# Optimization experiments

Measured on AMD Instinct MI355X. Metric: run time of the kernel, lower is better.

The kernel has to match this reference:

```python
import jax, jax.numpy as jnp
import numpy as np

BITWIDTH = 4  # sqllm 4-bit packing: 8 codes per int32


def sqllm_dequant4(qweight, lut):
    # qweight: [num_int32s, N] int32 (stored packed); lut: [N, 16]
    qw = qweight.T  # [N, num_int32s]
    shifts = jnp.arange(8, dtype=jnp.int32) * 4  # [8]
    # extract 8 nibbles per int32 -> indices in [0, 16)
    idx = (qw[:, :, None] >> shifts[None, None, :]) & 15  # [N, num_int32s, 8]
    N = qw.shape[0]
    idx = idx.reshape(N, -1)  # [N, K] with K = num_int32s * 8
    return jnp.take_along_axis(lut, idx, axis=1)  # [N, K]


def setup_inputs() -> dict:
    key = jax.random.key(0)
    k1, k2, k3 = jax.random.split(key, 3)
    B, S, K, N = 4, 2048, 4096, 4096
    inp = {
        "input": jax.random.normal(k1, (B, S, K), dtype=jnp.float32),
        "qweight": jax.random.randint(k2, (K // 8, N), 0, 2147483647, dtype=jnp.int32),
        "lut": jax.random.normal(k3, (N, 16), dtype=jnp.float32),
    }
    return inp


def reference(input, qweight, lut):
    # sqllm_gemm: dequantize packed 4-bit weights via LUT gather, then input @ W.T
    weights = sqllm_dequant4(qweight, lut)  # [N, K]
    return jnp.einsum("bsk,nk->bsn", input, weights)  # [B, S, N]
```

## Files before the change

### kernel.cpp

```cpp
#include <hip/hip_runtime.h>
#include <hip/hip_bf16.h>


typedef __attribute__((ext_vector_type(4))) float  f32x4;
typedef __attribute__((ext_vector_type(4))) int    i32x4;
typedef __attribute__((ext_vector_type(8))) short  bf16x8;

__device__ __forceinline__ unsigned short f2bf(float f) {
    __hip_bfloat16 h = __float2bfloat16(f);
    return __builtin_bit_cast(unsigned short, h);
}

__device__ __forceinline__ void gload16(const unsigned short* g, unsigned short* l) {
    __builtin_amdgcn_global_load_lds(
        (const __attribute__((address_space(1))) unsigned int*)g,
        (__attribute__((address_space(3))) unsigned int*)l, 16, 0, 0);
}


__global__ void convA_kernel(const float* __restrict__ in, unsigned short* __restrict__ o, long n8) {
    long i = (long)blockIdx.x * blockDim.x + threadIdx.x;
    long stride = (long)gridDim.x * blockDim.x;
    const f32x4* in4 = reinterpret_cast<const f32x4*>(in);
    bf16x8* o8 = reinterpret_cast<bf16x8*>(o);
    for (; i < n8; i += stride) {
        f32x4 a = in4[2 * i];
        f32x4 b = in4[2 * i + 1];
        bf16x8 e;
#pragma unroll
        for (int x = 0; x < 4; ++x) {
            e[x]     = (short)f2bf(a[x]);
            e[4 + x] = (short)f2bf(b[x]);
        }
        o8[i] = e;
    }
}

__global__ void dequantW_kernel(const int* __restrict__ Q, const float* __restrict__ lut,
                                unsigned short* __restrict__ Wb, int N, long total) {
    long i = (long)blockIdx.x * blockDim.x + threadIdx.x;
    if (i >= total) return;
    unsigned int v = (unsigned int)Q[i];
    int n = (int)(i % N);
    const float* lp = lut + (long)n * 16;
    bf16x8 w;
#pragma unroll
    for (int p = 0; p < 8; ++p)
        w[p] = (short)f2bf(lp[(v >> (4 * p)) & 15]);
    reinterpret_cast<bf16x8*>(Wb)[i] = w;
}


__global__ __launch_bounds__(512, 2)
void gemm8p(const unsigned short* __restrict__ Abf, const unsigned short* __restrict__ Wb,
            float* __restrict__ out, int M, int N, int K) {
    __shared__ __align__(16) unsigned short sA[4 * 8192];
    __shared__ __align__(16) unsigned short sB[4 * 8192];

    const int tid  = threadIdx.x;
    const int lane = tid & 63;
    const int wid  = tid >> 6;
    const int wr   = wid >> 2;
    const int wc   = wid & 3;
    const int r15  = lane & 15;
    const int hi   = lane >> 4;

    int nwg = gridDim.x, orig = blockIdx.x;
    int wg = ((nwg & 7) == 0) ? (orig & 7) * (nwg >> 3) + (orig >> 3) : orig;
    const int NBN = N / 256;
    const int m0 = (wg / NBN) * 256, n0 = (wg % NBN) * 256;

    const int NH = K / 32;

    const int aoff = (wr * 128 + r15) * 32 + ((hi ^ ((r15 >> 1) & 3)) << 3);
    const int boff = hi * 2048 + (wc * 64 + r15) * 8;

    auto stage = [&](int S, int slot) {
#pragma unroll
        for (int j = 0; j < 2; ++j) {
            int idx = j * 512 + tid;
            int m = idx >> 2, kc = idx & 3;
            const unsigned short* srcA = Abf + (size_t)(m0 + m) * K + S * 32
                                         + ((kc ^ ((m >> 1) & 3)) << 3);
            gload16(srcA, sA + slot * 8192 + j * 4096 + wid * 512);
            int kc2 = idx >> 8, n = idx & 255;
            const unsigned short* srcB = Wb + ((size_t)(S * 4 + kc2) * N + n0 + n) * 8;
            gload16(srcB, sB + slot * 8192 + j * 4096 + wid * 512);
        }
    };

    f32x4 acc[8][4] = {};

    stage(0, 0);
    stage(1, 1);
    stage(2, 2);
    asm volatile("s_waitcnt vmcnt(8)" ::: "memory");
    __builtin_amdgcn_s_barrier();

#define PHASE(U) do {                                                             \
    const unsigned short* SA = sA + (U) * 8192;                                   \
    const unsigned short* SB = sB + (U) * 8192;                                   \
    bf16x8 av[8], bv[4];                                                          \
    _Pragma("unroll") for (int nf = 0; nf < 4; ++nf)                              \
        bv[nf] = *(const bf16x8*)(SB + boff + nf * 128);                          \
    _Pragma("unroll") for (int mf = 0; mf < 8; ++mf)                              \
        av[mf] = *(const bf16x8*)(SA + aoff + mf * 512);                          \
    int S = H + (U) + 3; if (S >= NH) S -= NH;                                    \
    stage(S, ((U) + 3) & 3);                                                      \
    asm volatile("s_waitcnt vmcnt(8)" ::: "memory");                              \
    __builtin_amdgcn_s_barrier();                                                 \
    __builtin_amdgcn_s_setprio(1);                                                \
    _Pragma("unroll") for (int mf = 0; mf < 8; ++mf)                              \
        _Pragma("unroll") for (int nf = 0; nf < 4; ++nf)                          \
            acc[mf][nf] = __builtin_amdgcn_mfma_f32_16x16x32_bf16(                \
                av[mf], bv[nf], acc[mf][nf], 0, 0, 0);                            \
    __builtin_amdgcn_s_setprio(0);                                                \
    __builtin_amdgcn_s_barrier();                                                 \
} while (0)

    for (int H = 0; H < NH; H += 4) {
        PHASE(0);
        PHASE(1);
        PHASE(2);
        PHASE(3);
    }
#undef PHASE

    asm volatile("s_waitcnt vmcnt(0)" ::: "memory");

#pragma unroll
    for (int mf = 0; mf < 8; ++mf) {
        const int mrow = m0 + wr * 128 + mf * 16 + hi * 4;
#pragma unroll
        for (int nf = 0; nf < 4; ++nf) {
            const int ncol = n0 + wc * 64 + nf * 16 + r15;
            float* po = out + (size_t)mrow * N + ncol;
#pragma unroll
            for (int r = 0; r < 4; ++r) po[(size_t)r * N] = acc[mf][nf][r];
        }
    }
}


#define FBM 128
#define FBN 128
#define FBK 64

__device__ __forceinline__ int fswz(int row, int kb) {
    return row * (FBK * 2) + (kb ^ ((row & 7) << 4));
}

__global__ __launch_bounds__(256, 2)
void sqllm_gemm_fused(const float* __restrict__ A, const int* __restrict__ Q,
                      const float* __restrict__ lut, float* __restrict__ out,
                      int M, int N, int K) {
    __shared__ __align__(16) char sA[FBM * FBK * 2];
    __shared__ __align__(16) char sB[FBN * FBK * 2];
    __shared__ float sLut[FBN * 17];

    const int tid  = threadIdx.x;
    const int lane = tid & 63;
    const int wid  = tid >> 6;
    const int wr   = wid >> 1;
    const int wc   = wid & 1;
    const int n0 = blockIdx.x * FBN;
    const int m0 = blockIdx.y * FBM;

    for (int i = tid; i < FBN * 16; i += 256) {
        int n = i >> 4, c = i & 15;
        sLut[n * 17 + c] = lut[(long)(n0 + n) * 16 + c];
    }
    __syncthreads();

    f32x4 acc[4][4] = {};
    const int nK = K / FBK;
    for (int kk = 0; kk < nK; ++kk) {
        {
            const int r = tid >> 1, h = tid & 1;
            const float* ap = A + (long)(m0 + r) * K + kk * FBK + h * 32;
            f32x4 v[8];
#pragma unroll
            for (int j = 0; j < 8; ++j) v[j] = reinterpret_cast<const f32x4*>(ap)[j];
            const int kr = tid >> 5, nq = (tid & 31) << 2;
            const int* qp = Q + (long)(kk * (FBK / 8) + kr) * N + n0 + nq;
            i32x4 q = *reinterpret_cast<const i32x4*>(qp);
#pragma unroll
            for (int j = 0; j < 4; ++j) {
                bf16x8 e;
#pragma unroll
                for (int x = 0; x < 4; ++x) {
                    e[x]     = (short)f2bf(v[2 * j][x]);
                    e[4 + x] = (short)f2bf(v[2 * j + 1][x]);
                }
                *reinterpret_cast<bf16x8*>(sA + fswz(r, h * 64 + j * 16)) = e;
            }
#pragma unroll
            for (int c = 0; c < 4; ++c) {
                const int n = nq + c;
                const float* lp = sLut + n * 17;
                unsigned int qq = (unsigned int)q[c];
                bf16x8 w;
#pragma unroll
                for (int p = 0; p < 8; ++p)
                    w[p] = (short)f2bf(lp[(qq >> (4 * p)) & 15]);
                *reinterpret_cast<bf16x8*>(sB + fswz(n, kr * 16)) = w;
            }
        }
        __syncthreads();
#pragma unroll
        for (int kh = 0; kh < 2; ++kh) {
            const int kb = kh * 64 + (lane >> 4) * 16;
            bf16x8 af[4], bfv[4];
#pragma unroll
            for (int i = 0; i < 4; ++i) {
                af[i]  = *reinterpret_cast<const bf16x8*>(sA + fswz(wr * 64 + i * 16 + (lane & 15), kb));
                bfv[i] = *reinterpret_cast<const bf16x8*>(sB + fswz(wc * 64 + i * 16 + (lane & 15), kb));
            }
#pragma unroll
            for (int i = 0; i < 4; ++i)
#pragma unroll
                for (int j = 0; j < 4; ++j)
                    acc[i][j] = __builtin_amdgcn_mfma_f32_16x16x32_bf16(af[i], bfv[j], acc[i][j], 0, 0, 0);
        }
        __syncthreads();
    }
    const int col = lane & 15;
    const int r4  = (lane >> 4) * 4;
#pragma unroll
    for (int i = 0; i < 4; ++i) {
        const int mrow = m0 + wr * 64 + i * 16 + r4;
#pragma unroll
        for (int j = 0; j < 4; ++j) {
            const int ncol = n0 + wc * 64 + j * 16 + col;
#pragma unroll
            for (int r = 0; r < 4; ++r)
                out[(long)(mrow + r) * N + ncol] = acc[i][j][r];
        }
    }
}

extern "C" void kernel_launch(void* const* d_in, const int* in_sizes, int n_in,
                              void* d_out, int out_size, void* d_ws, size_t ws_size,
                              hipStream_t stream) {
    const float* A   = (const float*)d_in[0];
    const int*   Q   = (const int*)d_in[1];
    const float* lut = (const float*)d_in[2];
    float* out = (float*)d_out;

    const long szA = in_sizes[0], szQ = in_sizes[1], szL = in_sizes[2];
    const int N = (int)(szL / 16);
    const int K = (int)(szQ * 8 / N);
    const int M = (int)(szA / K);

    const size_t needA = (size_t)M * K * 2;
    const size_t needW = (size_t)K * N * 2;

    const bool shape_ok = (M % 256 == 0) && (N % 256 == 0) && (K % 128 == 0);

    if (shape_ok && ws_size >= needA + needW) {
        unsigned short* Abf = (unsigned short*)d_ws;
        unsigned short* Wb  = (unsigned short*)((char*)d_ws + needA);
        const long n8 = (long)M * K / 8;
        convA_kernel<<<2048, 256, 0, stream>>>(A, Abf, n8);
        const long tq = (long)(K / 8) * N;
        dequantW_kernel<<<(int)((tq + 255) / 256), 256, 0, stream>>>(Q, lut, Wb, N, tq);
        dim3 grid((M / 256) * (N / 256));
        gemm8p<<<grid, 512, 0, stream>>>(Abf, Wb, out, M, N, K);
    } else {
        dim3 grid(N / FBN, M / FBM);
        sqllm_gemm_fused<<<grid, 256, 0, stream>>>(A, Q, lut, out, M, N, K);
    }
}
```

Baseline: 299.5 us.

## Interleave LDS fragment loads with MFMAs and drop mid-phase barrier

Precomputes per-thread global source and LDS destination pointers so each stage issue is four loads with simple offsets instead of recomputed index math. The phase body now issues the next stage's prefetch first, then interleaves the A-fragment LDS reads with the MFMA groups so that matrix ops start before all fragments are loaded. It also removes one of the two barriers per phase by moving the vmcnt wait and single barrier to the end. This lowers register pressure and address-arithmetic overhead, but relies on the 4-slot ring leaving enough distance that dropping the barrier does not create LDS read/write races.

```diff
diff --git a/kernel.cpp b/kernel.cpp
--- a/kernel.cpp
+++ b/kernel.cpp
@@ -51,6 +51,12 @@
 }
 
 
+#define MFMA4(MF, AF) \
+    acc[MF][0] = __builtin_amdgcn_mfma_f32_16x16x32_bf16(AF, bv0, acc[MF][0], 0, 0, 0); \
+    acc[MF][1] = __builtin_amdgcn_mfma_f32_16x16x32_bf16(AF, bv1, acc[MF][1], 0, 0, 0); \
+    acc[MF][2] = __builtin_amdgcn_mfma_f32_16x16x32_bf16(AF, bv2, acc[MF][2], 0, 0, 0); \
+    acc[MF][3] = __builtin_amdgcn_mfma_f32_16x16x32_bf16(AF, bv3, acc[MF][3], 0, 0, 0);
+
 __global__ __launch_bounds__(512, 2)
 void gemm8p(const unsigned short* __restrict__ Abf, const unsigned short* __restrict__ Wb,
             float* __restrict__ out, int M, int N, int K) {
@@ -75,18 +81,22 @@
     const int aoff = (wr * 128 + r15) * 32 + ((hi ^ ((r15 >> 1) & 3)) << 3);
     const int boff = hi * 2048 + (wc * 64 + r15) * 8;
 
+    const int am  = tid >> 2, akc = tid & 3;
+    const int akcs = (akc ^ ((am >> 1) & 3)) << 3;
+    const unsigned short* baseA0 = Abf + (size_t)(m0 + am) * K + akcs;
+    const unsigned short* baseA1 = Abf + (size_t)(m0 + am + 128) * K + akcs;
+    const int bkc = tid >> 8, bn = tid & 255;
+    const unsigned short* baseB0 = Wb + ((size_t)bkc * N + n0 + bn) * 8;
+    const unsigned short* baseB1 = Wb + ((size_t)(bkc + 2) * N + n0 + bn) * 8;
+    const size_t bstride = (size_t)32 * N;
+    unsigned short* const dA = sA + wid * 512;
+    unsigned short* const dB = sB + wid * 512;
+
     auto stage = [&](int S, int slot) {
-#pragma unroll
-        for (int j = 0; j < 2; ++j) {
-            int idx = j * 512 + tid;
-            int m = idx >> 2, kc = idx & 3;
-            const unsigned short* srcA = Abf + (size_t)(m0 + m) * K + S * 32
-                                         + ((kc ^ ((m >> 1) & 3)) << 3);
-            gload16(srcA, sA + slot * 8192 + j * 4096 + wid * 512);
-            int kc2 = idx >> 8, n = idx & 255;
-            const unsigned short* srcB = Wb + ((size_t)(S * 4 + kc2) * N + n0 + n) * 8;
-            gload16(srcB, sB + slot * 8192 + j * 4096 + wid * 512);
-        }
+        gload16(baseA0 + S * 32, dA + slot * 8192);
+        gload16(baseB0 + S * bstride, dB + slot * 8192);
+        gload16(baseA1 + S * 32, dA + slot * 8192 + 4096);
+        gload16(baseB1 + S * bstride, dB + slot * 8192 + 4096);
     };
 
     f32x4 acc[8][4] = {};
@@ -100,21 +110,31 @@
 #define PHASE(U) do {                                                             \
     const unsigned short* SA = sA + (U) * 8192;                                   \
     const unsigned short* SB = sB + (U) * 8192;                                   \
-    bf16x8 av[8], bv[4];                                                          \
-    _Pragma("unroll") for (int nf = 0; nf < 4; ++nf)                              \
-        bv[nf] = *(const bf16x8*)(SB + boff + nf * 128);                          \
-    _Pragma("unroll") for (int mf = 0; mf < 8; ++mf)                              \
-        av[mf] = *(const bf16x8*)(SA + aoff + mf * 512);                          \
     int S = H + (U) + 3; if (S >= NH) S -= NH;                                    \
     stage(S, ((U) + 3) & 3);                                                      \
+    bf16x8 bv0 = *(const bf16x8*)(SB + boff + 0 * 128);                           \
+    bf16x8 bv1 = *(const bf16x8*)(SB + boff + 1 * 128);                           \
+    bf16x8 bv2 = *(const bf16x8*)(SB + boff + 2 * 128);                           \
+    bf16x8 bv3 = *(const bf16x8*)(SB + boff + 3 * 128);                           \
+    bf16x8 a0 = *(const bf16x8*)(SA + aoff + 0 * 512);                            \
+    bf16x8 a1 = *(const bf16x8*)(SA + aoff + 1 * 512);                            \
+    __builtin_amdgcn_s_setprio(1);                                                \
+    bf16x8 a2 = *(const bf16x8*)(SA + aoff + 2 * 512);                            \
+    bf16x8 a3 = *(const bf16x8*)(SA + aoff + 3 * 512);                            \
+    MFMA4(0, a0)                                                                  \
+    MFMA4(1, a1)                                                                  \
+    bf16x8 a4 = *(const bf16x8*)(SA + aoff + 4 * 512);                            \
+    bf16x8 a5 = *(const bf16x8*)(SA + aoff + 5 * 512);                            \
+    MFMA4(2, a2)                                                                  \
+    MFMA4(3, a3)                                                                  \
+    bf16x8 a6 = *(const bf16x8*)(SA + aoff + 6 * 512);                            \
+    bf16x8 a7 = *(const bf16x8*)(SA + aoff + 7 * 512);                            \
+    MFMA4(4, a4)                                                                  \
+    MFMA4(5, a5)                                                                  \
+    MFMA4(6, a6)                                                                  \
+    MFMA4(7, a7)                                                                  \
+    __builtin_amdgcn_s_setprio(0);                                                \
     asm volatile("s_waitcnt vmcnt(8)" ::: "memory");                              \
-    __builtin_amdgcn_s_barrier();                                                 \
-    __builtin_amdgcn_s_setprio(1);                                                \
-    _Pragma("unroll") for (int mf = 0; mf < 8; ++mf)                              \
-        _Pragma("unroll") for (int nf = 0; nf < 4; ++nf)                          \
-            acc[mf][nf] = __builtin_amdgcn_mfma_f32_16x16x32_bf16(                \
-                av[mf], bv[nf], acc[mf][nf], 0, 0, 0);                            \
-    __builtin_amdgcn_s_setprio(0);                                                \
     __builtin_amdgcn_s_barrier();                                                 \
 } while (0)
 
```

New measurement: 295.7 us. No clear change (-1.3%).

## Replace 256x256 GEMM tile with 256x128 tile, 4 waves, triple-buffered pipeline

Applied to the files above, without the earlier changes.

The main bf16 GEMM moves from 512-thread blocks with 256x256 output tiles and a 4-slot LDS ring to 256-thread blocks with 256x128 tiles and a 3-slot ring. The K loop is now a single rolled loop with one barrier per step instead of two, and global load addresses are precomputed outside the loop. The aim is lower LDS use and sync overhead and more blocks in flight. The trade-off is that a smaller N tile lowers reuse of A per block, so more A traffic goes to global memory.

```diff
diff --git a/kernel.cpp b/kernel.cpp
--- a/kernel.cpp
+++ b/kernel.cpp
@@ -51,80 +51,87 @@
 }
 
 
-__global__ __launch_bounds__(512, 2)
-void gemm8p(const unsigned short* __restrict__ Abf, const unsigned short* __restrict__ Wb,
+__global__ __launch_bounds__(256, 2)
+void gemm2b(const unsigned short* __restrict__ Abf, const unsigned short* __restrict__ Wb,
             float* __restrict__ out, int M, int N, int K) {
-    __shared__ __align__(16) unsigned short sA[4 * 8192];
-    __shared__ __align__(16) unsigned short sB[4 * 8192];
+    __shared__ __align__(16) unsigned short sA[3 * 8192];
+    __shared__ __align__(16) unsigned short sB[3 * 4096];
 
     const int tid  = threadIdx.x;
     const int lane = tid & 63;
     const int wid  = tid >> 6;
-    const int wr   = wid >> 2;
-    const int wc   = wid & 3;
+    const int wr   = wid >> 1;
+    const int wc   = wid & 1;
     const int r15  = lane & 15;
     const int hi   = lane >> 4;
 
+    const int NBN = N / 128;
     int nwg = gridDim.x, orig = blockIdx.x;
     int wg = ((nwg & 7) == 0) ? (orig & 7) * (nwg >> 3) + (orig >> 3) : orig;
-    const int NBN = N / 256;
-    const int m0 = (wg / NBN) * 256, n0 = (wg % NBN) * 256;
+    const int m0 = (wg / NBN) * 256, n0 = (wg % NBN) * 128;
 
     const int NH = K / 32;
 
     const int aoff = (wr * 128 + r15) * 32 + ((hi ^ ((r15 >> 1) & 3)) << 3);
-    const int boff = hi * 2048 + (wc * 64 + r15) * 8;
+    const int boff = hi * 1024 + (wc * 64 + r15) * 8;
+
+    const int am  = tid >> 2, akc = tid & 3;
+    const int akcs = (akc ^ ((am >> 1) & 3)) << 3;
+    const unsigned short* baseA = Abf + (size_t)(m0 + am) * K + akcs;
+    const size_t ajump = (size_t)64 * K;
+    const int bn = tid & 127, bk0 = tid >> 7;
+    const unsigned short* baseB0 = Wb + ((size_t)bk0 * N + n0 + bn) * 8;
+    const unsigned short* baseB1 = Wb + ((size_t)(bk0 + 2) * N + n0 + bn) * 8;
+    const size_t bstride = (size_t)32 * N;
+    unsigned short* const dA = sA + wid * 512;
+    unsigned short* const dB = sB + wid * 512;
 
     auto stage = [&](int S, int slot) {
-#pragma unroll
-        for (int j = 0; j < 2; ++j) {
-            int idx = j * 512 + tid;
-            int m = idx >> 2, kc = idx & 3;
-            const unsigned short* srcA = Abf + (size_t)(m0 + m) * K + S * 32
-                                         + ((kc ^ ((m >> 1) & 3)) << 3);
-            gload16(srcA, sA + slot * 8192 + j * 4096 + wid * 512);
-            int kc2 = idx >> 8, n = idx & 255;
-            const unsigned short* srcB = Wb + ((size_t)(S * 4 + kc2) * N + n0 + n) * 8;
-            gload16(srcB, sB + slot * 8192 + j * 4096 + wid * 512);
-        }
+        const unsigned short* a = baseA + (size_t)S * 32;
+        unsigned short* da = dA + slot * 8192;
+#pragma unroll
+        for (int j = 0; j < 4; ++j)
+            gload16(a + j * ajump, da + j * 2048);
+        gload16(baseB0 + S * bstride, dB + slot * 4096);
+        gload16(baseB1 + S * bstride, dB + slot * 4096 + 2048);
     };
 
     f32x4 acc[8][4] = {};
 
     stage(0, 0);
     stage(1, 1);
-    stage(2, 2);
-    asm volatile("s_waitcnt vmcnt(8)" ::: "memory");
+    asm volatile("s_waitcnt vmcnt(6)" ::: "memory");
     __builtin_amdgcn_s_barrier();
 
-#define PHASE(U) do {                                                             \
-    const unsigned short* SA = sA + (U) * 8192;                                   \
-    const unsigned short* SB = sB + (U) * 8192;                                   \
-    bf16x8 av[8], bv[4];                                                          \
-    _Pragma("unroll") for (int nf = 0; nf < 4; ++nf)                              \
-        bv[nf] = *(const bf16x8*)(SB + boff + nf * 128);                          \
-    _Pragma("unroll") for (int mf = 0; mf < 8; ++mf)                              \
-        av[mf] = *(const bf16x8*)(SA + aoff + mf * 512);                          \
-    int S = H + (U) + 3; if (S >= NH) S -= NH;                                    \
-    stage(S, ((U) + 3) & 3);                                                      \
-    asm volatile("s_waitcnt vmcnt(8)" ::: "memory");                              \
-    __builtin_amdgcn_s_barrier();                                                 \
-    __builtin_amdgcn_s_setprio(1);                                                \
-    _Pragma("unroll") for (int mf = 0; mf < 8; ++mf)                              \
-        _Pragma("unroll") for (int nf = 0; nf < 4; ++nf)                          \
-            acc[mf][nf] = __builtin_amdgcn_mfma_f32_16x16x32_bf16(                \
-                av[mf], bv[nf], acc[mf][nf], 0, 0, 0);                            \
-    __builtin_amdgcn_s_setprio(0);                                                \
-    __builtin_amdgcn_s_barrier();                                                 \
-} while (0)
-
-    for (int H = 0; H < NH; H += 4) {
-        PHASE(0);
-        PHASE(1);
-        PHASE(2);
-        PHASE(3);
-    }
-#undef PHASE
+    int cur = 0, stg = 2;
+    for (int h = 0; h < NH; ++h) {
+        int S = h + 2; if (S >= NH) S -= NH;
+        stage(S, stg);
+
+        const unsigned short* SA = sA + cur * 8192;
+        const unsigned short* SB = sB + cur * 4096;
+        bf16x8 bv[4], av[8];
+#pragma unroll
+        for (int nf = 0; nf < 4; ++nf)
+            bv[nf] = *(const bf16x8*)(SB + boff + nf * 128);
+#pragma unroll
+        for (int mf = 0; mf < 8; ++mf)
+            av[mf] = *(const bf16x8*)(SA + aoff + mf * 512);
+
+        __builtin_amdgcn_s_setprio(1);
+#pragma unroll
+        for (int mf = 0; mf < 8; ++mf)
+#pragma unroll
+            for (int nf = 0; nf < 4; ++nf)
+                acc[mf][nf] = __builtin_amdgcn_mfma_f32_16x16x32_bf16(
+                    av[mf], bv[nf], acc[mf][nf], 0, 0, 0);
+        __builtin_amdgcn_s_setprio(0);
+
+        asm volatile("s_waitcnt vmcnt(6)" ::: "memory");
+        __builtin_amdgcn_s_barrier();
+        cur = (cur == 2) ? 0 : cur + 1;
+        stg = (stg == 2) ? 0 : stg + 1;
+    }
 
     asm volatile("s_waitcnt vmcnt(0)" ::: "memory");
 
@@ -255,7 +262,7 @@
     const size_t needA = (size_t)M * K * 2;
     const size_t needW = (size_t)K * N * 2;
 
-    const bool shape_ok = (M % 256 == 0) && (N % 256 == 0) && (K % 128 == 0);
+    const bool shape_ok = (M % 256 == 0) && (N % 128 == 0) && (K % 64 == 0);
 
     if (shape_ok && ws_size >= needA + needW) {
         unsigned short* Abf = (unsigned short*)d_ws;
@@ -264,8 +271,8 @@
         convA_kernel<<<2048, 256, 0, stream>>>(A, Abf, n8);
         const long tq = (long)(K / 8) * N;
         dequantW_kernel<<<(int)((tq + 255) / 256), 256, 0, stream>>>(Q, lut, Wb, N, tq);
-        dim3 grid((M / 256) * (N / 256));
-        gemm8p<<<grid, 512, 0, stream>>>(Abf, Wb, out, M, N, K);
+        dim3 grid((M / 256) * (N / 128));
+        gemm2b<<<grid, 256, 0, stream>>>(Abf, Wb, out, M, N, K);
     } else {
         dim3 grid(N / FBN, M / FBM);
         sqllm_gemm_fused<<<grid, 256, 0, stream>>>(A, Q, lut, out, M, N, K);
```

Measured after the change: 316.7 us. 5.7% more time.

## Drop LDS staging in GEMM; load MFMA fragments directly from K-chunked bf16 A layout

Applied to the files above, without the earlier changes.

The A conversion kernel now writes bf16 activations in a K-chunked layout (32-wide K chunks, row-major within a chunk), so each lane's MFMA fragment is a contiguous 16-byte global load. The GEMM no longer stages tiles through shared memory with barriers. Each wave instead loads its A and B fragments straight from global memory into registers, double-buffered across K chunks. This removes LDS traffic and workgroup syncs, but every wave now re-reads data its neighbours also need, relying on cache for reuse and leaving load latency exposed without the deeper multi-stage pipeline.

```diff
diff --git a/kernel.cpp b/kernel.cpp
--- a/kernel.cpp
+++ b/kernel.cpp
@@ -11,28 +11,27 @@
     return __builtin_bit_cast(unsigned short, h);
 }
 
-__device__ __forceinline__ void gload16(const unsigned short* g, unsigned short* l) {
-    __builtin_amdgcn_global_load_lds(
-        (const __attribute__((address_space(1))) unsigned int*)g,
-        (__attribute__((address_space(3))) unsigned int*)l, 16, 0, 0);
-}
-
-
-__global__ void convA_kernel(const float* __restrict__ in, unsigned short* __restrict__ o, long n8) {
+
+__global__ void convA2_kernel(const float* __restrict__ in, unsigned short* __restrict__ o,
+                              int M, int K) {
+    const long total = (long)M * (K / 8);
     long i = (long)blockIdx.x * blockDim.x + threadIdx.x;
-    long stride = (long)gridDim.x * blockDim.x;
-    const f32x4* in4 = reinterpret_cast<const f32x4*>(in);
-    bf16x8* o8 = reinterpret_cast<bf16x8*>(o);
-    for (; i < n8; i += stride) {
-        f32x4 a = in4[2 * i];
-        f32x4 b = in4[2 * i + 1];
+    const long stride = (long)gridDim.x * blockDim.x;
+    const int K8 = K / 8;
+    for (; i < total; i += stride) {
+        const long m = i / K8;
+        const long k0 = (i % K8) * 8;
+        const f32x4* src = reinterpret_cast<const f32x4*>(in + m * K + k0);
+        f32x4 a = src[0];
+        f32x4 b = src[1];
         bf16x8 e;
 #pragma unroll
         for (int x = 0; x < 4; ++x) {
             e[x]     = (short)f2bf(a[x]);
             e[4 + x] = (short)f2bf(b[x]);
         }
-        o8[i] = e;
+        const long kc = k0 >> 5, ko = k0 & 31;
+        reinterpret_cast<bf16x8*>(o)[(kc * M + m) * 4 + (ko >> 3)] = e;
     }
 }
 
@@ -51,12 +50,15 @@
 }
 
 
+#define MFMABLOCK(CA, CB)                                                         \
+    _Pragma("unroll") for (int mf = 0; mf < 8; ++mf)                              \
+        _Pragma("unroll") for (int nf = 0; nf < 4; ++nf)                          \
+            acc[mf][nf] = __builtin_amdgcn_mfma_f32_16x16x32_bf16(                \
+                CA[mf], CB[nf], acc[mf][nf], 0, 0, 0);
+
 __global__ __launch_bounds__(512, 2)
-void gemm8p(const unsigned short* __restrict__ Abf, const unsigned short* __restrict__ Wb,
-            float* __restrict__ out, int M, int N, int K) {
-    __shared__ __align__(16) unsigned short sA[4 * 8192];
-    __shared__ __align__(16) unsigned short sB[4 * 8192];
-
+void gemm_nolds(const unsigned short* __restrict__ Abf2, const unsigned short* __restrict__ Wb,
+                float* __restrict__ out, int M, int N, int K) {
     const int tid  = threadIdx.x;
     const int lane = tid & 63;
     const int wid  = tid >> 6;
@@ -65,68 +67,45 @@
     const int r15  = lane & 15;
     const int hi   = lane >> 4;
 
+    const int NBN = N / 256;
     int nwg = gridDim.x, orig = blockIdx.x;
     int wg = ((nwg & 7) == 0) ? (orig & 7) * (nwg >> 3) + (orig >> 3) : orig;
-    const int NBN = N / 256;
     const int m0 = (wg / NBN) * 256, n0 = (wg % NBN) * 256;
 
-    const int NH = K / 32;
-
-    const int aoff = (wr * 128 + r15) * 32 + ((hi ^ ((r15 >> 1) & 3)) << 3);
-    const int boff = hi * 2048 + (wc * 64 + r15) * 8;
-
-    auto stage = [&](int S, int slot) {
-#pragma unroll
-        for (int j = 0; j < 2; ++j) {
-            int idx = j * 512 + tid;
-            int m = idx >> 2, kc = idx & 3;
-            const unsigned short* srcA = Abf + (size_t)(m0 + m) * K + S * 32
-                                         + ((kc ^ ((m >> 1) & 3)) << 3);
-            gload16(srcA, sA + slot * 8192 + j * 4096 + wid * 512);
-            int kc2 = idx >> 8, n = idx & 255;
-            const unsigned short* srcB = Wb + ((size_t)(S * 4 + kc2) * N + n0 + n) * 8;
-            gload16(srcB, sB + slot * 8192 + j * 4096 + wid * 512);
-        }
-    };
+    const int KC = K / 32;
+
+    const bf16x8* pA = reinterpret_cast<const bf16x8*>(
+        Abf2 + (size_t)(m0 + wr * 128 + r15) * 32 + hi * 8);
+    const size_t aChunk = (size_t)M * 4;
+    const bf16x8* pB = reinterpret_cast<const bf16x8*>(
+        Wb + ((size_t)hi * N + n0 + wc * 64 + r15) * 8);
+    const size_t bChunk = (size_t)N * 4;
 
     f32x4 acc[8][4] = {};
-
-    stage(0, 0);
-    stage(1, 1);
-    stage(2, 2);
-    asm volatile("s_waitcnt vmcnt(8)" ::: "memory");
-    __builtin_amdgcn_s_barrier();
-
-#define PHASE(U) do {                                                             \
-    const unsigned short* SA = sA + (U) * 8192;                                   \
-    const unsigned short* SB = sB + (U) * 8192;                                   \
-    bf16x8 av[8], bv[4];                                                          \
-    _Pragma("unroll") for (int nf = 0; nf < 4; ++nf)                              \
-        bv[nf] = *(const bf16x8*)(SB + boff + nf * 128);                          \
-    _Pragma("unroll") for (int mf = 0; mf < 8; ++mf)                              \
-        av[mf] = *(const bf16x8*)(SA + aoff + mf * 512);                          \
-    int S = H + (U) + 3; if (S >= NH) S -= NH;                                    \
-    stage(S, ((U) + 3) & 3);                                                      \
-    asm volatile("s_waitcnt vmcnt(8)" ::: "memory");                              \
-    __builtin_amdgcn_s_barrier();                                                 \
-    __builtin_amdgcn_s_setprio(1);                                                \
-    _Pragma("unroll") for (int mf = 0; mf < 8; ++mf)                              \
-        _Pragma("unroll") for (int nf = 0; nf < 4; ++nf)                          \
-            acc[mf][nf] = __builtin_amdgcn_mfma_f32_16x16x32_bf16(                \
-                av[mf], bv[nf], acc[mf][nf], 0, 0, 0);                            \
-    __builtin_amdgcn_s_setprio(0);                                                \
-    __builtin_amdgcn_s_barrier();                                                 \
+    bf16x8 a0[8], b0[4], a1[8], b1[4];
+
+#define LOADA(BUF, C) do {                                                        \
+    const bf16x8* ba_ = pA + (size_t)(C) * aChunk;                                \
+    _Pragma("unroll") for (int mf = 0; mf < 8; ++mf) BUF[mf] = ba_[mf * 64];      \
 } while (0)
-
-    for (int H = 0; H < NH; H += 4) {
-        PHASE(0);
-        PHASE(1);
-        PHASE(2);
-        PHASE(3);
-    }
-#undef PHASE
-
-    asm volatile("s_waitcnt vmcnt(0)" ::: "memory");
+#define LOADB(BUF, C) do {                                                        \
+    const bf16x8* bb_ = pB + (size_t)(C) * bChunk;                                \
+    _Pragma("unroll") for (int nf = 0; nf < 4; ++nf) BUF[nf] = bb_[nf * 16];      \
+} while (0)
+
+    LOADA(a0, 0); LOADB(b0, 0);
+    for (int c = 0; c + 2 < KC; c += 2) {
+        LOADA(a1, c + 1); LOADB(b1, c + 1);
+        MFMABLOCK(a0, b0)
+        LOADA(a0, c + 2); LOADB(b0, c + 2);
+        MFMABLOCK(a1, b1)
+    }
+    LOADA(a1, KC - 1); LOADB(b1, KC - 1);
+    MFMABLOCK(a0, b0)
+    MFMABLOCK(a1, b1)
+
+#undef LOADA
+#undef LOADB
 
 #pragma unroll
     for (int mf = 0; mf < 8; ++mf) {
@@ -140,6 +119,8 @@
         }
     }
 }
+
+#undef MFMABLOCK
 
 
 #define FBM 128
@@ -255,17 +236,16 @@
     const size_t needA = (size_t)M * K * 2;
     const size_t needW = (size_t)K * N * 2;
 
-    const bool shape_ok = (M % 256 == 0) && (N % 256 == 0) && (K % 128 == 0);
+    const bool shape_ok = (M % 256 == 0) && (N % 256 == 0) && (K % 64 == 0);
 
     if (shape_ok && ws_size >= needA + needW) {
-        unsigned short* Abf = (unsigned short*)d_ws;
-        unsigned short* Wb  = (unsigned short*)((char*)d_ws + needA);
-        const long n8 = (long)M * K / 8;
-        convA_kernel<<<2048, 256, 0, stream>>>(A, Abf, n8);
+        unsigned short* Abf2 = (unsigned short*)d_ws;
+        unsigned short* Wb   = (unsigned short*)((char*)d_ws + needA);
+        convA2_kernel<<<2048, 256, 0, stream>>>(A, Abf2, M, K);
         const long tq = (long)(K / 8) * N;
         dequantW_kernel<<<(int)((tq + 255) / 256), 256, 0, stream>>>(Q, lut, Wb, N, tq);
         dim3 grid((M / 256) * (N / 256));
-        gemm8p<<<grid, 512, 0, stream>>>(Abf, Wb, out, M, N, K);
+        gemm_nolds<<<grid, 512, 0, stream>>>(Abf2, Wb, out, M, N, K);
     } else {
         dim3 grid(N / FBN, M / FBM);
         sqllm_gemm_fused<<<grid, 256, 0, stream>>>(A, Q, lut, out, M, N, K);
```

Result: slower. 371.3 us (+24.0%).
